# Kernel optimization log

Hardware: AMD Instinct MI355X
Metric: run time of the kernel (lower is better)

## Reference

```python
import jax, jax.numpy as jnp
import numpy as np

B, S, IN_DIM, EMBED, H = 2, 2048, 512, 512, 8
HD = EMBED // H


def setup_inputs() -> dict:
    key = jax.random.key(0)
    ks = jax.random.split(key, 6)
    x = jax.random.normal(ks[0], (B, S, IN_DIM), dtype=jnp.float32)
    dist_mat = jax.random.normal(ks[1], (B, H, S, S), dtype=jnp.float32) * 0.02
    path_mat = jax.random.normal(ks[2], (B, H, S, S), dtype=jnp.float32) * 0.02
    # xavier-uniform-style init scale
    qkv_w = jax.random.normal(ks[3], (IN_DIM, 3 * EMBED), dtype=jnp.float32) * (1.0 / np.sqrt(IN_DIM))
    qkv_b = jnp.zeros((3 * EMBED,), dtype=jnp.float32)
    o_w = jax.random.normal(ks[4], (EMBED, EMBED), dtype=jnp.float32) * (1.0 / np.sqrt(EMBED))
    o_b = jnp.zeros((EMBED,), dtype=jnp.float32)
    return {"x": x, "dist_mat": dist_mat, "path_mat": path_mat,
            "qkv_w": qkv_w, "qkv_b": qkv_b, "o_w": o_w, "o_b": o_b}


def reference(x, dist_mat, path_mat, qkv_w, qkv_b, o_w, o_b):
    b, s, _ = x.shape
    qkv = x @ qkv_w + qkv_b                         # [B,S,3*EMBED]
    qkv = qkv.reshape(b, s, H, 3 * HD).transpose(0, 2, 1, 3)  # [B,H,S,3*HD]
    q, k, v = jnp.split(qkv, 3, axis=-1)            # each [B,H,S,HD]
    logits = jnp.einsum('bhqd,bhkd->bhqk', q, k) / jnp.sqrt(jnp.float32(HD))
    attn = jax.nn.softmax(logits, axis=-1)
    attn = attn + dist_mat + path_mat               # post-softmax bias (breaks flash fusion)
    vals = jnp.einsum('bhqk,bhkd->bhqd', attn, v)   # [B,H,S,HD]
    vals = vals.transpose(0, 2, 1, 3).reshape(b, s, EMBED)
    return vals @ o_w + o_b
```

## Files before the change

kernel.cpp:

```cpp
#include <hip/hip_runtime.h>
#include <stdint.h>
#include <stddef.h>

#define B_ 2
#define H_ 8
#define S_ 2048
#define D_ 64
#define E_ 512
#define N3_ 1536
#define M_ (B_*S_)
#define K_ 512

typedef __attribute__((ext_vector_type(4))) float f32x4;
typedef __attribute__((ext_vector_type(8))) __bf16 bf16x8;
typedef __attribute__((ext_vector_type(4))) __bf16 bf16x4;

static __device__ __forceinline__ int swz(int b) { return b ^ (((b >> 7) & 7) << 4); }

static __device__ __forceinline__ void gl_lds16(const void* g, void* l) {
    __builtin_amdgcn_global_load_lds((const __attribute__((address_space(1))) void*)g,
                                     (__attribute__((address_space(3))) void*)l, 16, 0, 0);
}

__global__ void cvt_bf16_kernel(const float* __restrict__ in, __bf16* __restrict__ out, int n4) {
    int i = blockIdx.x * blockDim.x + threadIdx.x;
    if (i < n4) {
        float4 v = reinterpret_cast<const float4*>(in)[i];
        bf16x4 o;
        o[0] = (__bf16)v.x; o[1] = (__bf16)v.y; o[2] = (__bf16)v.z; o[3] = (__bf16)v.w;
        reinterpret_cast<bf16x4*>(out)[i] = o;
    }
}

__global__ void transpose_cvt_kernel(const float* __restrict__ in, __bf16* __restrict__ out,
                                     int R, int C) {
    __shared__ float tile[32][33];
    int tc = blockIdx.x * 32, tr = blockIdx.y * 32;
    int lx = threadIdx.x & 31, ly = threadIdx.x >> 5;
    #pragma unroll
    for (int p = 0; p < 4; ++p) {
        int r = tr + ly + p * 8, c = tc + lx;
        if (r < R && c < C) tile[ly + p * 8][lx] = in[(size_t)r * C + c];
    }
    __syncthreads();
    #pragma unroll
    for (int p = 0; p < 4; ++p) {
        int oc = tc + ly + p * 8;
        int orow = tr + lx;
        if (oc < C && orow < R) out[(size_t)oc * R + orow] = (__bf16)tile[lx][ly + p * 8];
    }
}

__global__ void transpose_v_kernel(const __bf16* __restrict__ v, __bf16* __restrict__ vt) {
    __shared__ __bf16 t[64][65];
    int bh = blockIdx.x >> 5;
    int s0 = (blockIdx.x & 31) << 6;
    int tid = threadIdx.x;
    const __bf16* src = v + ((size_t)bh * S_ + s0) * D_;
    #pragma unroll
    for (int p = 0; p < 2; ++p) {
        int idx = (p * 256 + tid) * 8;
        int r = idx >> 6, c = idx & 63;
        bf16x8 val = *reinterpret_cast<const bf16x8*>(src + (size_t)r * D_ + c);
        #pragma unroll
        for (int e = 0; e < 8; ++e) t[r][c + e] = val[e];
    }
    __syncthreads();
    __bf16* dst = vt + (size_t)bh * D_ * S_ + s0;
    #pragma unroll
    for (int p = 0; p < 16; ++p) {
        int idx = p * 256 + tid;
        int d = idx >> 6, s = idx & 63;
        dst[(size_t)d * S_ + s] = t[s][d];
    }
}

template<int MODE>
__global__ __launch_bounds__(256, 2) void gemm_kernel(
    const __bf16* __restrict__ A, const __bf16* __restrict__ Bt,
    const float* __restrict__ bias,
    void* __restrict__ o0, void* __restrict__ o1, void* __restrict__ o2,
    int M, int N, int K)
{
    __shared__ __align__(16) __bf16 lA[128 * 64];
    __shared__ __align__(16) __bf16 lB[128 * 64];
    const int tid = threadIdx.x;
    const int wave = tid >> 6, lane = tid & 63;
    const int wm = wave >> 1, wn = wave & 1;
    const int m0 = blockIdx.y * 128, n0 = blockIdx.x * 128;
    const int l15 = lane & 15, l4 = lane >> 4;

    f32x4 acc[4][4] = {};

    for (int k0 = 0; k0 < K; k0 += 64) {
        __syncthreads();
        #pragma unroll
        for (int p = 0; p < 4; ++p) {
            int base = p * 4096 + wave * 1024;
            int js = swz(base + lane * 16);
            int row = js >> 7, colb = js & 127;
            gl_lds16((const char*)A + ((size_t)(m0 + row) * K + k0) * 2 + colb, (char*)lA + base);
            gl_lds16((const char*)Bt + ((size_t)(n0 + row) * K + k0) * 2 + colb, (char*)lB + base);
        }
        __syncthreads();
        #pragma unroll
        for (int ks = 0; ks < 2; ++ks) {
            bf16x8 af[4], bfr[4];
            #pragma unroll
            for (int i = 0; i < 4; ++i) {
                af[i]  = *(const bf16x8*)((const char*)lA + swz(((wm * 64 + i * 16 + l15) << 7) + ks * 64 + (l4 << 4)));
                bfr[i] = *(const bf16x8*)((const char*)lB + swz(((wn * 64 + i * 16 + l15) << 7) + ks * 64 + (l4 << 4)));
            }
            #pragma unroll
            for (int i = 0; i < 4; ++i)
                #pragma unroll
                for (int j = 0; j < 4; ++j)
                    acc[i][j] = __builtin_amdgcn_mfma_f32_16x16x32_bf16(af[i], bfr[j], acc[i][j], 0, 0, 0);
        }
    }
    #pragma unroll
    for (int i = 0; i < 4; ++i) {
        int mg0 = m0 + wm * 64 + i * 16 + (l4 << 2);
        #pragma unroll
        for (int j = 0; j < 4; ++j) {
            int ng = n0 + wn * 64 + j * 16 + l15;
            float bv = bias[ng];
            #pragma unroll
            for (int r = 0; r < 4; ++r) {
                int m = mg0 + r;
                float val = acc[i][j][r] + bv;
                if (MODE == 0) {
                    int h = ng / 192, rr = ng % 192;
                    int which = rr >> 6, d = rr & 63;
                    int b = m >> 11, s = m & (S_ - 1);
                    if (which == 0) val *= 0.125f;
                    __bf16* dst = which == 0 ? (__bf16*)o0 : which == 1 ? (__bf16*)o1 : (__bf16*)o2;
                    dst[(((size_t)((b * H_ + h) * S_ + s)) << 6) + d] = (__bf16)val;
                } else {
                    ((float*)o0)[(size_t)m * N + ng] = val;
                }
            }
        }
    }
}

__global__ __launch_bounds__(256, 1) void attn_kernel(
    const __bf16* __restrict__ q, const __bf16* __restrict__ k,
    const __bf16* __restrict__ vt,
    const float* __restrict__ dist, const float* __restrict__ path,
    __bf16* __restrict__ vals)
{
    __shared__ __align__(16) __bf16 kl[2][64 * 64];
    __shared__ __align__(16) __bf16 vl[2][64 * 64];
    __shared__ __align__(16) __bf16 pl[4][16 * 64];
    __shared__ __align__(16) float  bl[2][2][4][1024];
    const int tid = threadIdx.x, wave = tid >> 6, lane = tid & 63;
    const int l15 = lane & 15, l4 = lane >> 4;
    const int id = blockIdx.x;
    const int xcd = id & 7, j = id >> 3;
    const int bh = xcd * 2 + (j >> 5);
    const int q0 = (j & 31) << 6;
    const int b = bh >> 3, h = bh & 7;
    const int qrow = q0 + wave * 16 + l15;

    const __bf16* qp = q + ((size_t)bh * S_ + qrow) * D_;
    bf16x8 qf0 = *(const bf16x8*)(qp + (l4 << 3));
    bf16x8 qf1 = *(const bf16x8*)(qp + 32 + (l4 << 3));

    const char* dg = (const char*)(dist + (size_t)bh * S_ * S_);
    const char* pg = (const char*)(path + (size_t)bh * S_ * S_);
    const char* kg = (const char*)(k + (size_t)bh * S_ * D_);
    const char* vg = (const char*)(vt + (size_t)bh * D_ * S_);

    auto STAGE = [&](int kt, int buf) {
        #pragma unroll
        for (int p = 0; p < 2; ++p) {
            int base = p * 4096 + wave * 1024;
            int js = swz(base + lane * 16);
            int row = js >> 7, colb = js & 127;
            gl_lds16(kg + ((size_t)(kt + row) * D_) * 2 + colb, (char*)kl[buf] + base);
            gl_lds16(vg + ((size_t)row * S_ + kt) * 2 + colb, (char*)vl[buf] + base);
        }
        #pragma unroll
        for (int p = 0; p < 4; ++p) {
            int jj = p * 64 + lane;
            int row = jj >> 4;
            int csrc = (jj & 15) ^ (row & 7);
            size_t goff = ((size_t)(q0 + wave * 16 + row) * S_ + kt) * 4 + csrc * 16;
            gl_lds16(dg + goff, (char*)&bl[buf][0][wave][0] + jj * 16);
            gl_lds16(pg + goff, (char*)&bl[buf][1][wave][0] + jj * 16);
        }
    };

    float m_run[4], l_run[4];
    f32x4 o_p[4] = {}, o_b[4] = {};
    #pragma unroll
    for (int r = 0; r < 4; ++r) { m_run[r] = -1e30f; l_run[r] = 0.f; }

    STAGE(0, 0);
    __syncthreads();

    int cur = 0;
    #pragma unroll 1
    for (int kt = 0; kt < S_; kt += 64) {
        int ktn = (kt + 64 < S_) ? kt + 64 : kt;
        STAGE(ktn, cur ^ 1);
        __builtin_amdgcn_sched_barrier(0);

        bf16x8 ba[2];
        {
            const char* dl = (const char*)&bl[cur][0][wave][0];
            const char* plp = (const char*)&bl[cur][1][wave][0];
            #pragma unroll
            for (int ks = 0; ks < 2; ++ks) {
                int c0 = ks * 8 + (l4 << 1);
                int a0 = (l15 * 16 + (c0 ^ (l15 & 7))) * 16;
                int a1 = (l15 * 16 + ((c0 + 1) ^ (l15 & 7))) * 16;
                f32x4 d0 = *(const f32x4*)(dl + a0);
                f32x4 d1 = *(const f32x4*)(dl + a1);
                f32x4 p0 = *(const f32x4*)(plp + a0);
                f32x4 p1 = *(const f32x4*)(plp + a1);
                ba[ks][0] = (__bf16)(d0[0] + p0[0]); ba[ks][1] = (__bf16)(d0[1] + p0[1]);
                ba[ks][2] = (__bf16)(d0[2] + p0[2]); ba[ks][3] = (__bf16)(d0[3] + p0[3]);
                ba[ks][4] = (__bf16)(d1[0] + p1[0]); ba[ks][5] = (__bf16)(d1[1] + p1[1]);
                ba[ks][6] = (__bf16)(d1[2] + p1[2]); ba[ks][7] = (__bf16)(d1[3] + p1[3]);
            }
        }

        f32x4 lg[4] = {};
        #pragma unroll
        for (int ks = 0; ks < 2; ++ks) {
            bf16x8 qa = ks ? qf1 : qf0;
            #pragma unroll
            for (int n = 0; n < 4; ++n) {
                bf16x8 kf = *(const bf16x8*)((const char*)kl[cur] + swz(((n * 16 + l15) << 7) + ks * 64 + (l4 << 4)));
                lg[n] = __builtin_amdgcn_mfma_f32_16x16x32_bf16(qa, kf, lg[n], 0, 0, 0);
            }
        }
        #pragma unroll
        for (int ks = 0; ks < 2; ++ks)
            #pragma unroll
            for (int n = 0; n < 4; ++n) {
                bf16x8 vf = *(const bf16x8*)((const char*)vl[cur] + swz(((n * 16 + l15) << 7) + ks * 64 + (l4 << 4)));
                o_b[n] = __builtin_amdgcn_mfma_f32_16x16x32_bf16(ba[ks], vf, o_b[n], 0, 0, 0);
            }
        float scale[4], rsum[4], pe[4][4];
        #pragma unroll
        for (int r = 0; r < 4; ++r) {
            float t = fmaxf(fmaxf(lg[0][r], lg[1][r]), fmaxf(lg[2][r], lg[3][r]));
            t = fmaxf(t, __shfl_xor(t, 1));
            t = fmaxf(t, __shfl_xor(t, 2));
            t = fmaxf(t, __shfl_xor(t, 4));
            t = fmaxf(t, __shfl_xor(t, 8));
            float mnew = fmaxf(m_run[r], t);
            scale[r] = __expf(m_run[r] - mnew);
            m_run[r] = mnew;
            rsum[r] = 0.f;
        }
        #pragma unroll
        for (int n = 0; n < 4; ++n)
            #pragma unroll
            for (int r = 0; r < 4; ++r) {
                pe[n][r] = __expf(lg[n][r] - m_run[r]);
                rsum[r] += pe[n][r];
            }
        #pragma unroll
        for (int r = 0; r < 4; ++r) {
            float s = rsum[r];
            s += __shfl_xor(s, 1);
            s += __shfl_xor(s, 2);
            s += __shfl_xor(s, 4);
            s += __shfl_xor(s, 8);
            l_run[r] = l_run[r] * scale[r] + s;
        }
        #pragma unroll
        for (int n = 0; n < 4; ++n)
            #pragma unroll
            for (int r = 0; r < 4; ++r)
                o_p[n][r] *= scale[r];
        char* pb = (char*)&pl[wave][0];
        #pragma unroll
        for (int n = 0; n < 4; ++n)
            #pragma unroll
            for (int r = 0; r < 4; ++r) {
                int prow = (l4 << 2) + r, pcol = n * 16 + l15;
                *(__bf16*)(pb + swz((prow << 7) + pcol * 2)) = (__bf16)pe[n][r];
            }
        #pragma unroll
        for (int ks = 0; ks < 2; ++ks) {
            bf16x8 pa = *(const bf16x8*)((const char*)pb + swz((l15 << 7) + ks * 64 + (l4 << 4)));
            #pragma unroll
            for (int n = 0; n < 4; ++n) {
                bf16x8 vf = *(const bf16x8*)((const char*)vl[cur] + swz(((n * 16 + l15) << 7) + ks * 64 + (l4 << 4)));
                o_p[n] = __builtin_amdgcn_mfma_f32_16x16x32_bf16(pa, vf, o_p[n], 0, 0, 0);
            }
        }
        __syncthreads();
        cur ^= 1;
    }
    #pragma unroll
    for (int r = 0; r < 4; ++r) {
        int s = q0 + wave * 16 + (l4 << 2) + r;
        float inv = 1.f / l_run[r];
        __bf16* dst = vals + (size_t)(b * S_ + s) * E_ + h * D_;
        #pragma unroll
        for (int n = 0; n < 4; ++n) {
            int d = n * 16 + l15;
            dst[d] = (__bf16)(o_p[n][r] * inv + o_b[n][r]);
        }
    }
}

extern "C" void kernel_launch(void* const* d_in, const int* in_sizes, int n_in,
                              void* d_out, int out_size, void* d_ws, size_t ws_size,
                              hipStream_t stream) {
    (void)in_sizes; (void)n_in; (void)out_size; (void)ws_size;
    const float* x      = (const float*)d_in[0];
    const float* dist   = (const float*)d_in[1];
    const float* path   = (const float*)d_in[2];
    const float* qkv_w  = (const float*)d_in[3];
    const float* qkv_b  = (const float*)d_in[4];
    const float* o_w    = (const float*)d_in[5];
    const float* o_b    = (const float*)d_in[6];
    float* out = (float*)d_out;

    char* ws = (char*)d_ws;
    __bf16* xb     = (__bf16*)(ws);
    __bf16* qkv_wT = (__bf16*)(ws + (4  << 20));
    __bf16* o_wT   = (__bf16*)(ws + (6  << 20));
    __bf16* qb     = (__bf16*)(ws + (7  << 20));
    __bf16* kb     = (__bf16*)(ws + (11 << 20));
    __bf16* vb     = (__bf16*)(ws + (15 << 20));
    __bf16* vtb    = (__bf16*)(ws + (19 << 20));
    __bf16* valsb  = (__bf16*)(ws + (23 << 20));

    cvt_bf16_kernel<<<(M_ * K_ / 4 + 255) / 256, 256, 0, stream>>>(x, xb, M_ * K_ / 4);
    transpose_cvt_kernel<<<dim3(N3_ / 32, K_ / 32), 256, 0, stream>>>(qkv_w, qkv_wT, K_, N3_);
    transpose_cvt_kernel<<<dim3(E_ / 32, E_ / 32), 256, 0, stream>>>(o_w, o_wT, E_, E_);
    gemm_kernel<0><<<dim3(N3_ / 128, M_ / 128), 256, 0, stream>>>(xb, qkv_wT, qkv_b, qb, kb, vb, M_, N3_, K_);
    transpose_v_kernel<<<B_ * H_ * (S_ / 64), 256, 0, stream>>>(vb, vtb);
    attn_kernel<<<B_ * H_ * (S_ / 64), 256, 0, stream>>>(qb, kb, vtb, dist, path, valsb);
    gemm_kernel<1><<<dim3(E_ / 128, M_ / 128), 256, 0, stream>>>(valsb, o_wT, o_b, out, nullptr, nullptr, M_, E_, K_);
}
```

Before: 211.5 us.

## Load K/V fragments directly from global into registers, drop LDS staging

K and V tiles are no longer staged in LDS through async global-to-LDS copies. Each wave now reads its MFMA operand fragments for K and V straight from global memory into registers, and launch bounds are raised to two blocks per CU. The aim is to cut LDS footprint and traffic so more blocks fit per CU, leaving LDS only for the dist/path bias tiles and the probability buffer. The trade-off is that each of the four waves redundantly fetches the same K/V data from global/L2, and these loads are synchronous and not prefetched a tile ahead, so latency may be exposed.

```diff
diff --git a/kernel.cpp b/kernel.cpp
--- a/kernel.cpp
+++ b/kernel.cpp
@@ -144,16 +144,14 @@
     }
 }
 
-__global__ __launch_bounds__(256, 1) void attn_kernel(
+__global__ __launch_bounds__(256, 2) void attn_kernel(
     const __bf16* __restrict__ q, const __bf16* __restrict__ k,
     const __bf16* __restrict__ vt,
     const float* __restrict__ dist, const float* __restrict__ path,
     __bf16* __restrict__ vals)
 {
-    __shared__ __align__(16) __bf16 kl[2][64 * 64];
-    __shared__ __align__(16) __bf16 vl[2][64 * 64];
+    __shared__ __align__(16) float  bl[2][2][4][1024];
     __shared__ __align__(16) __bf16 pl[4][16 * 64];
-    __shared__ __align__(16) float  bl[2][2][4][1024];
     const int tid = threadIdx.x, wave = tid >> 6, lane = tid & 63;
     const int l15 = lane & 15, l4 = lane >> 4;
     const int id = blockIdx.x;
@@ -174,14 +172,6 @@
 
     auto STAGE = [&](int kt, int buf) {
         #pragma unroll
-        for (int p = 0; p < 2; ++p) {
-            int base = p * 4096 + wave * 1024;
-            int js = swz(base + lane * 16);
-            int row = js >> 7, colb = js & 127;
-            gl_lds16(kg + ((size_t)(kt + row) * D_) * 2 + colb, (char*)kl[buf] + base);
-            gl_lds16(vg + ((size_t)row * S_ + kt) * 2 + colb, (char*)vl[buf] + base);
-        }
-        #pragma unroll
         for (int p = 0; p < 4; ++p) {
             int jj = p * 64 + lane;
             int row = jj >> 4;
@@ -207,9 +197,18 @@
         STAGE(ktn, cur ^ 1);
         __builtin_amdgcn_sched_barrier(0);
 
+        bf16x8 kf[2][4], vf[2][4];
+        #pragma unroll
+        for (int ks = 0; ks < 2; ++ks)
+            #pragma unroll
+            for (int n = 0; n < 4; ++n) {
+                kf[ks][n] = *(const bf16x8*)(kg + (size_t)(kt + n * 16 + l15) * 128 + ks * 64 + (l4 << 4));
+                vf[ks][n] = *(const bf16x8*)(vg + (size_t)(n * 16 + l15) * (S_ * 2) + kt * 2 + ks * 64 + (l4 << 4));
+            }
+
         bf16x8 ba[2];
         {
-            const char* dl = (const char*)&bl[cur][0][wave][0];
+            const char* dl  = (const char*)&bl[cur][0][wave][0];
             const char* plp = (const char*)&bl[cur][1][wave][0];
             #pragma unroll
             for (int ks = 0; ks < 2; ++ks) {
@@ -232,18 +231,14 @@
         for (int ks = 0; ks < 2; ++ks) {
             bf16x8 qa = ks ? qf1 : qf0;
             #pragma unroll
-            for (int n = 0; n < 4; ++n) {
-                bf16x8 kf = *(const bf16x8*)((const char*)kl[cur] + swz(((n * 16 + l15) << 7) + ks * 64 + (l4 << 4)));
-                lg[n] = __builtin_amdgcn_mfma_f32_16x16x32_bf16(qa, kf, lg[n], 0, 0, 0);
-            }
+            for (int n = 0; n < 4; ++n)
+                lg[n] = __builtin_amdgcn_mfma_f32_16x16x32_bf16(qa, kf[ks][n], lg[n], 0, 0, 0);
         }
         #pragma unroll
         for (int ks = 0; ks < 2; ++ks)
             #pragma unroll
-            for (int n = 0; n < 4; ++n) {
-                bf16x8 vf = *(const bf16x8*)((const char*)vl[cur] + swz(((n * 16 + l15) << 7) + ks * 64 + (l4 << 4)));
-                o_b[n] = __builtin_amdgcn_mfma_f32_16x16x32_bf16(ba[ks], vf, o_b[n], 0, 0, 0);
-            }
+            for (int n = 0; n < 4; ++n)
+                o_b[n] = __builtin_amdgcn_mfma_f32_16x16x32_bf16(ba[ks], vf[ks][n], o_b[n], 0, 0, 0);
         float scale[4], rsum[4], pe[4][4];
         #pragma unroll
         for (int r = 0; r < 4; ++r) {
@@ -290,10 +285,8 @@
         for (int ks = 0; ks < 2; ++ks) {
             bf16x8 pa = *(const bf16x8*)((const char*)pb + swz((l15 << 7) + ks * 64 + (l4 << 4)));
             #pragma unroll
-            for (int n = 0; n < 4; ++n) {
-                bf16x8 vf = *(const bf16x8*)((const char*)vl[cur] + swz(((n * 16 + l15) << 7) + ks * 64 + (l4 << 4)));
-                o_p[n] = __builtin_amdgcn_mfma_f32_16x16x32_bf16(pa, vf, o_p[n], 0, 0, 0);
-            }
+            for (int n = 0; n < 4; ++n)
+                o_p[n] = __builtin_amdgcn_mfma_f32_16x16x32_bf16(pa, vf[ks][n], o_p[n], 0, 0, 0);
         }
         __syncthreads();
         cur ^= 1;
```

New measurement: 229.9 us. 8.7% more time.
